# Kernel optimization log

Hardware: AMD Instinct MI355X
Metric: run time of the kernel (lower is better)

## Reference

```python
import jax, jax.numpy as jnp
import numpy as np

N_NODES = 50000
N_EDGES = 800000
N_GRAPHS = 256
VOCAB = 40
EMB = 128
HID = 256
NCLS = 10


def setup_inputs() -> dict:
    key = jax.random.key(0)
    ks = jax.random.split(key, 12)
    x = jax.random.randint(ks[0], (N_NODES,), 0, VOCAB)
    edge_index = jax.random.randint(ks[1], (2, N_EDGES), 0, N_NODES)
    batch = jnp.sort(jax.random.randint(ks[2], (N_NODES,), 0, N_GRAPHS))

    def init(k, shape, fan_in):
        return jax.random.normal(k, shape, jnp.float32) * (1.0 / np.sqrt(fan_in))

    return {
        "x": x,
        "edge_index": edge_index,
        "batch": batch,
        "emb": init(ks[3], (VOCAB, EMB), EMB),
        "W1l": init(ks[4], (EMB, HID), EMB),
        "W1r": init(ks[5], (EMB, HID), EMB),
        "b1": jnp.zeros((HID,), jnp.float32),
        "W2l": init(ks[6], (HID, HID), HID),
        "W2r": init(ks[7], (HID, HID), HID),
        "b2": jnp.zeros((HID,), jnp.float32),
        "Wo": init(ks[8], (HID, NCLS), HID),
        "bo": jnp.zeros((NCLS,), jnp.float32),
    }


def _segment_mean(v, ids, n):
    # v: [M, D], ids: [M] -> [n, D] mean per segment (empty segments -> 0)
    s = jax.ops.segment_sum(v, ids, num_segments=n)
    c = jax.ops.segment_sum(jnp.ones((ids.shape[0], 1), v.dtype), ids, num_segments=n)
    return s / jnp.maximum(c, 1.0)


def _sage_conv(h, src, dst, Wl, Wr, b):
    # PyG SAGEConv: lin_l(mean of neighbor msgs) + lin_r(self) + bias
    mean_nb = _segment_mean(h[src], dst, h.shape[0])  # [N, D_in]
    return mean_nb @ Wl + h @ Wr + b


def reference(x, edge_index, batch, emb, W1l, W1r, b1, W2l, W2r, b2, Wo, bo):
    src, dst = edge_index[0], edge_index[1]
    h = emb[x]                                          # [N, EMB]
    h = jax.nn.relu(_sage_conv(h, src, dst, W1l, W1r, b1))  # [N, HID]
    h = jax.nn.relu(_sage_conv(h, src, dst, W2l, W2r, b2))  # [N, HID]
    g = _segment_mean(h, batch, N_GRAPHS)               # [G, HID]
    return g @ Wo + bo                                  # [G, NCLS]
```

## Files before the change

### kernel.cpp

```cpp
#include <hip/hip_runtime.h>
#include <hip/hip_bf16.h>

#define N_NODES 50000
#define N_GRAPHS 256
#define EMB 128
#define HID 256
#define NCLS 10
#define VOCAB 40
#define NPAD 50048
#define NROW 50048
#define DMAX 64
#define NEDGE 800000
#define P1B 64
#define EPB 12500

typedef __attribute__((ext_vector_type(4))) float f32x4;
typedef __attribute__((ext_vector_type(8))) _Float16 f16x8;
typedef __attribute__((ext_vector_type(4))) _Float16 f16x4;
typedef unsigned int u32;
#define AS1 __attribute__((address_space(1)))
#define AS3 __attribute__((address_space(3)))

__device__ __forceinline__ int imax(int a, int b) { return a > b ? a : b; }
__device__ __forceinline__ int imin(int a, int b) { return a < b ? a : b; }
__device__ __forceinline__ float bf2f(ushort h) { return __uint_as_float(((unsigned)h) << 16); }

__device__ __forceinline__ int detect_bf16(const unsigned short* w) {
    int ok = 1;
#pragma unroll
    for (int i = 0; i < 64; ++i) {
        float f = __uint_as_float(((unsigned)w[i]) << 16);
        ok &= (fabsf(f) < 16.0f) ? 1 : 0;
    }
    return ok;
}
__device__ __forceinline__ float ldw(const void* p, int idx, int bf) {
    if (bf) return bf2f(((const unsigned short*)p)[idx]);
    return ((const float*)p)[idx];
}


struct PrepArgs {
    const void* bsrc[4];
    const unsigned short* emb16;
    const void* W1l; const void* W1r;
    const void* W2l; const void* W2r;
    const int* batch;
    float* Wb;
    _Float16* W2t;
    _Float16* EWt;
    float* EW2;
    int* gstart;
    float* g_acc;
};

__global__ void prep_k(PrepArgs a) {
    int b = blockIdx.x, t = threadIdx.x;
    if (b < 13) {
        int i = b * 256 + t;
        if (i < 3082) {
            int bf = detect_bf16(a.emb16);
            const int cum[5] = {0, 256, 512, 3072, 3082};
            int s = 0;
            while (i >= cum[s + 1]) ++s;
            a.Wb[i] = ldw(a.bsrc[s], i - cum[s], bf);
        }
    } else if (b < 525) {
        int bf = detect_bf16(a.emb16);
        int j = (b - 13) * 256 + t;
        int n = j >> 9, k = j & 511;
        const void* p = (k < 256) ? a.W2l : a.W2r;
        a.W2t[(size_t)n * 512 + k] = (_Float16)ldw(p, (k & 255) * 256 + n, bf);
    } else if (b < 589) {
        int v = b - 525, n = t;
        if (v >= VOCAB) { a.EWt[n * 64 + v] = (_Float16)0.f; return; }
        int bf = detect_bf16(a.emb16);
        float s1 = 0.f, s2 = 0.f;
        for (int k = 0; k < EMB; ++k) {
            float ev = ldw(a.emb16, v * EMB + k, bf);
            s1 = fmaf(ev, ldw(a.W1l, k * 256 + n, bf), s1);
            s2 = fmaf(ev, ldw(a.W1r, k * 256 + n, bf), s2);
        }
        a.EWt[n * 64 + v] = (_Float16)s1;
        a.EW2[v * 256 + n] = s2;
    } else if (b < 785) {
        int i = (b - 589) * 256 + t;
        if (i < N_NODES) {
            int bb = a.batch[i];
            int bp = (i == 0) ? -1 : a.batch[i - 1];
            for (int g = bp + 1; g <= bb; ++g) a.gstart[g] = i;
            if (i == N_NODES - 1)
                for (int g = bb + 1; g <= N_GRAPHS; ++g) a.gstart[g] = N_NODES;
        }
    } else {
        int i = (b - 785) * 256 + t;
        if (i < N_GRAPHS * HID) a.g_acc[i] = 0.f;
    }
}

__global__ __launch_bounds__(1024) void p1_k(const int* __restrict__ dst,
                                             ushort* __restrict__ erank,
                                             ushort* __restrict__ cnts) {
    __shared__ u32 h[NROW / 2];
    int tid = threadIdx.x, blk = blockIdx.x;
    for (int w = tid; w < NROW / 2; w += 1024) h[w] = 0;
    __syncthreads();
    int base = blk * EPB;
    for (int i = tid; i < EPB; i += 1024) {
        int e = base + i;
        int d = dst[e];
        u32 sh = (u32)(d & 1) * 16u;
        u32 old = atomicAdd(&h[d >> 1], 1u << sh);
        erank[e] = (ushort)((old >> sh) & 0xffffu);
    }
    __syncthreads();
    u32* crow = (u32*)(cnts + (size_t)blk * NROW);
    for (int w = tid; w < NROW / 2; w += 1024) crow[w] = h[w];
}

__global__ __launch_bounds__(512) void p2_k(ushort* __restrict__ cnts,
                                            int* __restrict__ deg) {
    __shared__ ushort c[P1B][512];
    int t = threadIdx.x, nb = blockIdx.x * 512;
    int n = nb + t;
    bool ok = (n < NROW);
    for (int b = 0; b < P1B; ++b)
        c[b][t] = ok ? cnts[(size_t)b * NROW + n] : (ushort)0;
    int run = 0;
    for (int b = 0; b < P1B; ++b) {
        int v = c[b][t];
        c[b][t] = (ushort)run;
        run += v;
    }
    if (ok) {
        deg[n] = run;
        for (int b = 0; b < P1B; ++b) cnts[(size_t)b * NROW + n] = c[b][t];
    }
}

__global__ __launch_bounds__(1024) void p3_k(const int* __restrict__ src,
                                             const int* __restrict__ dst,
                                             const ushort* __restrict__ erank,
                                             const ushort* __restrict__ offs,
                                             ushort* __restrict__ col) {
    __shared__ ushort off_l[NROW];
    int tid = threadIdx.x, blk = blockIdx.x;
    const ushort* orow = offs + (size_t)blk * NROW;
    for (int w = tid; w < NROW; w += 1024) off_l[w] = orow[w];
    __syncthreads();
    int base = blk * EPB;
    for (int i = tid; i < EPB; i += 1024) {
        int e = base + i;
        int d = dst[e];
        int p = (int)off_l[d] + (int)erank[e];
        if (p < DMAX) col[(size_t)d * DMAX + p] = (ushort)src[e];
    }
}

__global__ void ct2_k(const int* __restrict__ deg, const ushort* __restrict__ colv,
                      const int* __restrict__ x, char* __restrict__ Ct) {
    __shared__ ushort cnt[VOCAB * 256];
    int tid = threadIdx.x;
    int nl = tid >> 2, sub = tid & 3;
    int n = blockIdx.x * 64 + nl;
#pragma unroll
    for (int v = 0; v < VOCAB; ++v) cnt[v * 256 + tid] = 0;
    if (n < N_NODES) {
        int s0 = n * DMAX;
        int s1 = s0 + imin(deg[n], DMAX);
        for (int e = s0 + sub; e < s1; e += 4) {
            int v = x[colv[e]];
            cnt[v * 256 + tid]++;
        }
    }
    __syncthreads();
    if (tid < 64) {
        int nn = blockIdx.x * 64 + tid;
        char* tile = Ct + (size_t)(nn >> 6) * 8192 + (nn & 63) * 128;
        int xorb = nn & 7;
#pragma unroll
        for (int b = 0; b < 8; ++b) {
            int kbase = (b ^ xorb) * 8;
            f16x8 o;
#pragma unroll
            for (int j = 0; j < 8; ++j) {
                int k = kbase + j;
                int c = 0;
                if (k < VOCAB)
                    c = cnt[k * 256 + tid * 4 + 0] + cnt[k * 256 + tid * 4 + 1] +
                        cnt[k * 256 + tid * 4 + 2] + cnt[k * 256 + tid * 4 + 3];
                o[j] = (_Float16)(float)c;
            }
            *(f16x8*)(tile + b * 16) = o;
        }
    }
}

__global__ __launch_bounds__(256, 2) void gemm1_k(
    const char* __restrict__ Ct, const _Float16* __restrict__ EWt,
    const float* __restrict__ EW2, const int* __restrict__ xv,
    const int* __restrict__ deg, const float* __restrict__ bias,
    char* __restrict__ E) {
    __shared__ __attribute__((aligned(16))) char As[8192];
    const int tid = threadIdx.x, wave = tid >> 6, lane = tid & 63;
    const int row0 = blockIdx.x * 64, col0 = wave * 64;
    const char* sp = Ct + (size_t)blockIdx.x * 8192 + tid * 16;
    __builtin_amdgcn_global_load_lds((const AS1 u32*)sp, (AS3 u32*)(As + tid * 16), 16, 0, 0);
    __builtin_amdgcn_global_load_lds((const AS1 u32*)(sp + 4096),
                                     (AS3 u32*)(As + tid * 16 + 4096), 16, 0, 0);
    f16x8 B[8];
#pragma unroll
    for (int n = 0; n < 4; ++n) {
        const _Float16* wp = EWt + (size_t)(col0 + n * 16 + (lane & 15)) * 64 + ((lane >> 4) * 8);
        B[n] = *(const f16x8*)wp;
        B[4 + n] = *(const f16x8*)(wp + 32);
    }
    int offA[2][4];
#pragma unroll
    for (int h = 0; h < 2; ++h)
#pragma unroll
        for (int m = 0; m < 4; ++m) {
            int r = (lane & 15) + m * 16;
            int b = h * 64 + (lane >> 4) * 16;
            offA[h][m] = r * 128 + (b ^ ((r & 7) << 4));
        }
    f32x4 acc[4][4];
#pragma unroll
    for (int m = 0; m < 4; ++m)
#pragma unroll
        for (int n = 0; n < 4; ++n) acc[m][n] = (f32x4){0.f, 0.f, 0.f, 0.f};
    asm volatile("s_waitcnt vmcnt(0)" ::: "memory");
    __syncthreads();
#pragma unroll
    for (int h = 0; h < 2; ++h) {
        f16x8 a[4];
#pragma unroll
        for (int m = 0; m < 4; ++m) a[m] = *(const f16x8*)(As + offA[h][m]);
#pragma unroll
        for (int m = 0; m < 4; ++m)
#pragma unroll
            for (int n = 0; n < 4; ++n)
                acc[m][n] = __builtin_amdgcn_mfma_f32_16x16x32_f16(a[m], B[h * 4 + n],
                                                                   acc[m][n], 0, 0, 0);
    }
    int rbase = row0 + ((lane >> 4) * 4);
    int cbase = col0 + (lane & 15);
    float bv[4];
#pragma unroll
    for (int n = 0; n < 4; ++n) bv[n] = bias[cbase + n * 16];
#pragma unroll
    for (int m = 0; m < 4; ++m)
#pragma unroll
        for (int r = 0; r < 4; ++r) {
            int row = rbase + m * 16 + r;
            if (row < N_NODES) {
                float invd = 1.f / (float)imax(deg[row], 1);
                const float* e2 = EW2 + (size_t)xv[row] * 256;
#pragma unroll
                for (int n = 0; n < 4; ++n) {
                    int colc = cbase + n * 16;
                    float v = acc[m][n][r] * invd + e2[colc] + bv[n];
                    v = v > 0.f ? v : 0.f;
                    char* ep = E + ((size_t)(row >> 6) * 8 + 4 + (colc >> 6)) * 8192 +
                               (row & 63) * 128 + (((colc & 63) * 2) ^ ((row & 7) << 4));
                    *(_Float16*)ep = (_Float16)v;
                }
            }
        }
}

__global__ void agg2_k(const int* __restrict__ deg, const ushort* __restrict__ colv,
                       char* __restrict__ A2c) {
    int w = (blockIdx.x * blockDim.x + threadIdx.x) >> 6;
    int lane = threadIdx.x & 63;
    if (w >= N_NODES) return;
    int dg = deg[w];
    int s0 = w * DMAX, s1 = s0 + imin(dg, DMAX);
    int ktof = 4 + (lane >> 4);
    int bof = (lane & 15) * 8;
    float ac0 = 0.f, ac1 = 0.f, ac2 = 0.f, ac3 = 0.f;
#define ADDR2(s) (A2c + ((size_t)((s) >> 6) * 8 + ktof) * 8192 + ((s) & 63) * 128 + \
                  (bof ^ (((s) & 7) << 4)))
    int e = s0;
    for (; e + 4 <= s1; e += 4) {
        int sA = colv[e], sB = colv[e + 1], sC = colv[e + 2], sD = colv[e + 3];
        f16x4 h0 = *(const f16x4*)ADDR2(sA);
        f16x4 h1 = *(const f16x4*)ADDR2(sB);
        f16x4 h2 = *(const f16x4*)ADDR2(sC);
        f16x4 h3 = *(const f16x4*)ADDR2(sD);
        ac0 += (float)h0[0] + (float)h1[0] + (float)h2[0] + (float)h3[0];
        ac1 += (float)h0[1] + (float)h1[1] + (float)h2[1] + (float)h3[1];
        ac2 += (float)h0[2] + (float)h1[2] + (float)h2[2] + (float)h3[2];
        ac3 += (float)h0[3] + (float)h1[3] + (float)h2[3] + (float)h3[3];
    }
    for (; e < s1; ++e) {
        f16x4 hv = *(const f16x4*)ADDR2(colv[e]);
        ac0 += (float)hv[0];
        ac1 += (float)hv[1];
        ac2 += (float)hv[2];
        ac3 += (float)hv[3];
    }
#undef ADDR2
    float inv = 1.f / (float)imax(dg, 1);
    f16x4 o;
    o[0] = (_Float16)(ac0 * inv);
    o[1] = (_Float16)(ac1 * inv);
    o[2] = (_Float16)(ac2 * inv);
    o[3] = (_Float16)(ac3 * inv);
    char* mp = A2c + ((size_t)(w >> 6) * 8 + (ktof - 4)) * 8192 + (w & 63) * 128 +
               (bof ^ ((w & 7) << 4));
    *(f16x4*)mp = o;
}

template <int K>
__global__ __launch_bounds__(256, 2) void gemm2_k(
    const char* __restrict__ Aswz, const _Float16* __restrict__ Wt,
    const float* __restrict__ bias, const int* __restrict__ batch,
    float* __restrict__ g_acc) {
    constexpr int NT = K / 64;
    __shared__ __attribute__((aligned(16))) char As[4 * 8192];
    const int tid = threadIdx.x, wave = tid >> 6, lane = tid & 63;
    const int row0 = blockIdx.x * 64, col0 = wave * 64;
    const char* Ab = Aswz + (size_t)blockIdx.x * NT * 8192 + tid * 16;
    const _Float16* Wp = Wt + (size_t)(col0 + (lane & 15)) * K + ((lane >> 4) * 8);

    int offA[2][4];
#pragma unroll
    for (int h = 0; h < 2; ++h)
#pragma unroll
        for (int m = 0; m < 4; ++m) {
            int r = (lane & 15) + m * 16;
            int b = h * 64 + (lane >> 4) * 16;
            offA[h][m] = r * 128 + (b ^ ((r & 7) << 4));
        }

    f32x4 acc[4][4];
#pragma unroll
    for (int m = 0; m < 4; ++m)
#pragma unroll
        for (int n = 0; n < 4; ++n) acc[m][n] = (f32x4){0.f, 0.f, 0.f, 0.f};

    f16x8 B0[8], B1[8];

#define STAGE(t)                                                                     \
    {                                                                                \
        const char* _s = Ab + (size_t)(t) * 8192;                                    \
        char* _d = As + ((t) & 3) * 8192 + tid * 16;                                 \
        __builtin_amdgcn_global_load_lds((const AS1 u32*)_s, (AS3 u32*)_d, 16, 0, 0);\
        __builtin_amdgcn_global_load_lds((const AS1 u32*)(_s + 4096),                \
                                         (AS3 u32*)(_d + 4096), 16, 0, 0);           \
    }
#define LOADB(t, Bf)                                                                 \
    {                                                                                \
        _Pragma("unroll") for (int n = 0; n < 4; ++n) {                              \
            Bf[n]     = *(const f16x8*)(Wp + (size_t)n * 16 * K + (t) * 64);         \
            Bf[4 + n] = *(const f16x8*)(Wp + (size_t)n * 16 * K + (t) * 64 + 32);    \
        }                                                                            \
    }
#define COMP(p, Bf)                                                                  \
    {                                                                                \
        const char* _b = As + (p) * 8192;                                            \
        _Pragma("unroll") for (int h = 0; h < 2; ++h) {                              \
            f16x8 _a[4];                                                             \
            _Pragma("unroll") for (int m = 0; m < 4; ++m)                            \
                _a[m] = *(const f16x8*)(_b + offA[h][m]);                            \
            _Pragma("unroll") for (int m = 0; m < 4; ++m)                            \
                _Pragma("unroll") for (int n = 0; n < 4; ++n)                        \
                    acc[m][n] = __builtin_amdgcn_mfma_f32_16x16x32_f16(              \
                        _a[m], Bf[h * 4 + n], acc[m][n], 0, 0, 0);                   \
        }                                                                            \
    }
#define WAITBAR()                                                                    \
    {                                                                                \
        asm volatile("s_waitcnt vmcnt(12)" ::: "memory");                            \
        __builtin_amdgcn_s_barrier();                                                \
        asm volatile("" ::: "memory");                                               \
    }

    STAGE(0);
    LOADB(0, B0);
    STAGE(1);
    STAGE(2);

#pragma unroll 1
    for (int t = 0; t < NT; t += 2) {
        WAITBAR();
        if (t + 3 < NT) STAGE(t + 3);
        LOADB(t + 1, B1);
        COMP(t & 3, B0);
        WAITBAR();
        if (t + 4 < NT) STAGE(t + 4);
        if (t + 2 < NT) LOADB(t + 2, B0);
        COMP((t + 1) & 3, B1);
    }

    __syncthreads();
    float bv[4];
#pragma unroll
    for (int n = 0; n < 4; ++n) bv[n] = bias[col0 + n * 16 + (lane & 15)];
    int rloc = (lane >> 4) * 4;
    int cbase = col0 + (lane & 15);
#pragma unroll
    for (int m = 0; m < 4; ++m)
#pragma unroll
        for (int n = 0; n < 4; ++n)
#pragma unroll
            for (int r = 0; r < 4; ++r) {
                float v = acc[m][n][r] + bv[n];
                v = v > 0.f ? v : 0.f;
                *(_Float16*)(As + (rloc + m * 16 + r) * 512 + (cbase + n * 16) * 2) =
                    (_Float16)v;
            }
    __syncthreads();
    int rmax = imin(64, N_NODES - row0);
    int cur = batch[row0];
    float run = 0.f;
    for (int r = 0; r < rmax; ++r) {
        int b = batch[row0 + r];
        if (b != cur) {
            atomicAdd(&g_acc[cur * HID + tid], run);
            run = 0.f;
            cur = b;
        }
        run += (float)*(const _Float16*)(As + r * 512 + tid * 2);
    }
    atomicAdd(&g_acc[cur * HID + tid], run);
#undef STAGE
#undef LOADB
#undef COMP
#undef WAITBAR
}

__global__ void final_k(const float* __restrict__ g_acc, const int* __restrict__ gstart,
                        const float* __restrict__ Wo, const float* __restrict__ bo,
                        void* __restrict__ out, const unsigned short* __restrict__ emb16) {
    __shared__ float gm[HID];
    __shared__ float red[HID];
    int g = blockIdx.x, t = threadIdx.x;
    int cnt = gstart[g + 1] - gstart[g];
    float inv = 1.0f / (float)imax(cnt, 1);
    gm[t] = g_acc[g * HID + t] * inv;
    __syncthreads();
    int bf = detect_bf16(emb16);
    for (int c = 0; c < NCLS; ++c) {
        red[t] = gm[t] * Wo[t * NCLS + c];
        __syncthreads();
        for (int s = HID / 2; s > 0; s >>= 1) {
            if (t < s) red[t] += red[t + s];
            __syncthreads();
        }
        if (t == 0) {
            float o = red[0] + bo[c];
            if (bf) ((__hip_bfloat16*)out)[g * NCLS + c] = __float2bfloat16(o);
            else    ((float*)out)[g * NCLS + c] = o;
        }
        __syncthreads();
    }
}

extern "C" void kernel_launch(void* const* d_in, const int* in_sizes, int n_in,
                              void* d_out, int out_size, void* d_ws, size_t ws_size,
                              hipStream_t stream) {
    const int* x     = (const int*)d_in[0];
    const int* ei    = (const int*)d_in[1];
    const int* batch = (const int*)d_in[2];
    const int* srcp = ei;
    const int* dstp = ei + NEDGE;

    char* w = (char*)d_ws;
    auto alloc = [&](size_t bytes) -> char* {
        char* p = w;
        w += (bytes + 255) & ~(size_t)255;
        return p;
    };
    float* g_acc = (float*)alloc((size_t)N_GRAPHS * HID * 4);
    int* deg     = (int*)alloc((size_t)NROW * 4);
    int* gstart  = (int*)alloc((size_t)(N_GRAPHS + 1) * 4);
    ushort* erank = (ushort*)alloc((size_t)NEDGE * 2);
    ushort* cnts  = (ushort*)alloc((size_t)P1B * NROW * 2);
    ushort* col   = (ushort*)alloc((size_t)N_NODES * DMAX * 2);
    float* Wb     = (float*)alloc((size_t)3328 * 4);
    _Float16* W2t = (_Float16*)alloc((size_t)256 * 512 * 2);
    _Float16* EWt = (_Float16*)alloc((size_t)256 * 64 * 2);
    float* EW2    = (float*)alloc((size_t)VOCAB * 256 * 4);
    char* Ct      = alloc((size_t)(NPAD / 64) * 8192);
    char* A2c     = alloc((size_t)(NPAD / 64) * 8 * 8192);
    alloc(4096);

    PrepArgs pa;
    pa.bsrc[0] = d_in[6];  pa.bsrc[1] = d_in[9];
    pa.bsrc[2] = d_in[10]; pa.bsrc[3] = d_in[11];
    pa.emb16 = (const unsigned short*)d_in[3];
    pa.W1l = d_in[4]; pa.W1r = d_in[5];
    pa.W2l = d_in[7]; pa.W2r = d_in[8];
    pa.batch = batch;
    pa.Wb = Wb; pa.W2t = W2t; pa.EWt = EWt; pa.EW2 = EW2;
    pa.gstart = gstart; pa.g_acc = g_acc;
    prep_k<<<1041, 256, 0, stream>>>(pa);

    p1_k<<<P1B, 1024, 0, stream>>>(dstp, erank, cnts);
    p2_k<<<(NROW + 511) / 512, 512, 0, stream>>>(cnts, deg);
    p3_k<<<P1B, 1024, 0, stream>>>(srcp, dstp, erank, cnts, col);

    const int GB = NPAD / 64;
    ct2_k<<<GB, 256, 0, stream>>>(deg, col, x, Ct);
    gemm1_k<<<GB, 256, 0, stream>>>(Ct, EWt, EW2, x, deg, Wb, A2c);
    agg2_k<<<(N_NODES * 64 + 255) / 256, 256, 0, stream>>>(deg, col, A2c);
    gemm2_k<512><<<GB, 256, 0, stream>>>(A2c, W2t, Wb + 256, batch, g_acc);
    final_k<<<N_GRAPHS, HID, 0, stream>>>(g_acc, gstart, Wb + 512, Wb + 3072, d_out,
                                          (const unsigned short*)d_in[3]);

    (void)in_sizes; (void)n_in; (void)out_size; (void)ws_size;
}
```

Measured before the change: 221.1 us.

## Replace multi-pass CSR build with atomic scatter and fuse vocab counts into gemm1

The three-kernel build of the neighbor lists (per-block histogram, prefix scan, placement) is replaced by one kernel. It uses a global atomicAdd on each node's degree to claim a slot and write the source id directly. The vocab-count kernel is merged into gemm1, so the count tile is built in LDS and consumed there without a global round trip. This removes three launches and the erank/cnts/Ct buffers. The cost is contended global atomics and a nondeterministic neighbor order.

```diff
diff --git a/kernel.cpp b/kernel.cpp
--- a/kernel.cpp
+++ b/kernel.cpp
@@ -8,11 +8,8 @@
 #define NCLS 10
 #define VOCAB 40
 #define NPAD 50048
-#define NROW 50048
 #define DMAX 64
 #define NEDGE 800000
-#define P1B 64
-#define EPB 12500
 
 typedef __attribute__((ext_vector_type(4))) float f32x4;
 typedef __attribute__((ext_vector_type(8))) _Float16 f16x8;
@@ -52,6 +49,7 @@
     float* EW2;
     int* gstart;
     float* g_acc;
+    int* deg;
 };
 
 __global__ void prep_k(PrepArgs a) {
@@ -92,79 +90,48 @@
             if (i == N_NODES - 1)
                 for (int g = bb + 1; g <= N_GRAPHS; ++g) a.gstart[g] = N_NODES;
         }
-    } else {
+    } else if (b < 1041) {
         int i = (b - 785) * 256 + t;
         if (i < N_GRAPHS * HID) a.g_acc[i] = 0.f;
-    }
-}
-
-__global__ __launch_bounds__(1024) void p1_k(const int* __restrict__ dst,
-                                             ushort* __restrict__ erank,
-                                             ushort* __restrict__ cnts) {
-    __shared__ u32 h[NROW / 2];
-    int tid = threadIdx.x, blk = blockIdx.x;
-    for (int w = tid; w < NROW / 2; w += 1024) h[w] = 0;
-    __syncthreads();
-    int base = blk * EPB;
-    for (int i = tid; i < EPB; i += 1024) {
-        int e = base + i;
+    } else {
+        int i = (b - 1041) * 256 + t;
+        if (i < N_NODES) a.deg[i] = 0;
+    }
+}
+
+__global__ void scatter_k(const int* __restrict__ src, const int* __restrict__ dst,
+                          int* __restrict__ deg, ushort* __restrict__ col) {
+    int e = blockIdx.x * blockDim.x + threadIdx.x;
+    if (e < NEDGE) {
         int d = dst[e];
-        u32 sh = (u32)(d & 1) * 16u;
-        u32 old = atomicAdd(&h[d >> 1], 1u << sh);
-        erank[e] = (ushort)((old >> sh) & 0xffffu);
-    }
-    __syncthreads();
-    u32* crow = (u32*)(cnts + (size_t)blk * NROW);
-    for (int w = tid; w < NROW / 2; w += 1024) crow[w] = h[w];
-}
-
-__global__ __launch_bounds__(512) void p2_k(ushort* __restrict__ cnts,
-                                            int* __restrict__ deg) {
-    __shared__ ushort c[P1B][512];
-    int t = threadIdx.x, nb = blockIdx.x * 512;
-    int n = nb + t;
-    bool ok = (n < NROW);
-    for (int b = 0; b < P1B; ++b)
-        c[b][t] = ok ? cnts[(size_t)b * NROW + n] : (ushort)0;
-    int run = 0;
-    for (int b = 0; b < P1B; ++b) {
-        int v = c[b][t];
-        c[b][t] = (ushort)run;
-        run += v;
-    }
-    if (ok) {
-        deg[n] = run;
-        for (int b = 0; b < P1B; ++b) cnts[(size_t)b * NROW + n] = c[b][t];
-    }
-}
-
-__global__ __launch_bounds__(1024) void p3_k(const int* __restrict__ src,
-                                             const int* __restrict__ dst,
-                                             const ushort* __restrict__ erank,
-                                             const ushort* __restrict__ offs,
-                                             ushort* __restrict__ col) {
-    __shared__ ushort off_l[NROW];
-    int tid = threadIdx.x, blk = blockIdx.x;
-    const ushort* orow = offs + (size_t)blk * NROW;
-    for (int w = tid; w < NROW; w += 1024) off_l[w] = orow[w];
-    __syncthreads();
-    int base = blk * EPB;
-    for (int i = tid; i < EPB; i += 1024) {
-        int e = base + i;
-        int d = dst[e];
-        int p = (int)off_l[d] + (int)erank[e];
-        if (p < DMAX) col[(size_t)d * DMAX + p] = (ushort)src[e];
-    }
-}
-
-__global__ void ct2_k(const int* __restrict__ deg, const ushort* __restrict__ colv,
-                      const int* __restrict__ x, char* __restrict__ Ct) {
+        int p = atomicAdd(&deg[d], 1);
+        if (p < DMAX) col[d * DMAX + p] = (ushort)src[e];
+    }
+}
+
+__global__ __launch_bounds__(256, 2) void gemm1_k(
+    const int* __restrict__ deg, const ushort* __restrict__ colv,
+    const int* __restrict__ x, const _Float16* __restrict__ EWt,
+    const float* __restrict__ EW2, const float* __restrict__ bias,
+    char* __restrict__ E) {
     __shared__ ushort cnt[VOCAB * 256];
-    int tid = threadIdx.x;
+    __shared__ __attribute__((aligned(16))) char As[8192];
+    const int tid = threadIdx.x, wave = tid >> 6, lane = tid & 63;
+    const int row0 = blockIdx.x * 64, col0 = wave * 64;
+
+    f16x8 B[8];
+#pragma unroll
+    for (int n = 0; n < 4; ++n) {
+        const _Float16* wp = EWt + (size_t)(col0 + n * 16 + (lane & 15)) * 64 + ((lane >> 4) * 8);
+        B[n] = *(const f16x8*)wp;
+        B[4 + n] = *(const f16x8*)(wp + 32);
+    }
+
     int nl = tid >> 2, sub = tid & 3;
-    int n = blockIdx.x * 64 + nl;
+    int n = row0 + nl;
 #pragma unroll
     for (int v = 0; v < VOCAB; ++v) cnt[v * 256 + tid] = 0;
+    __syncthreads();
     if (n < N_NODES) {
         int s0 = n * DMAX;
         int s1 = s0 + imin(deg[n], DMAX);
@@ -175,9 +142,8 @@
     }
     __syncthreads();
     if (tid < 64) {
-        int nn = blockIdx.x * 64 + tid;
-        char* tile = Ct + (size_t)(nn >> 6) * 8192 + (nn & 63) * 128;
-        int xorb = nn & 7;
+        char* trow = As + tid * 128;
+        int xorb = tid & 7;
 #pragma unroll
         for (int b = 0; b < 8; ++b) {
             int kbase = (b ^ xorb) * 8;
@@ -191,30 +157,11 @@
                         cnt[k * 256 + tid * 4 + 2] + cnt[k * 256 + tid * 4 + 3];
                 o[j] = (_Float16)(float)c;
             }
-            *(f16x8*)(tile + b * 16) = o;
-        }
-    }
-}
-
-__global__ __launch_bounds__(256, 2) void gemm1_k(
-    const char* __restrict__ Ct, const _Float16* __restrict__ EWt,
-    const float* __restrict__ EW2, const int* __restrict__ xv,
-    const int* __restrict__ deg, const float* __restrict__ bias,
-    char* __restrict__ E) {
-    __shared__ __attribute__((aligned(16))) char As[8192];
-    const int tid = threadIdx.x, wave = tid >> 6, lane = tid & 63;
-    const int row0 = blockIdx.x * 64, col0 = wave * 64;
-    const char* sp = Ct + (size_t)blockIdx.x * 8192 + tid * 16;
-    __builtin_amdgcn_global_load_lds((const AS1 u32*)sp, (AS3 u32*)(As + tid * 16), 16, 0, 0);
-    __builtin_amdgcn_global_load_lds((const AS1 u32*)(sp + 4096),
-                                     (AS3 u32*)(As + tid * 16 + 4096), 16, 0, 0);
-    f16x8 B[8];
-#pragma unroll
-    for (int n = 0; n < 4; ++n) {
-        const _Float16* wp = EWt + (size_t)(col0 + n * 16 + (lane & 15)) * 64 + ((lane >> 4) * 8);
-        B[n] = *(const f16x8*)wp;
-        B[4 + n] = *(const f16x8*)(wp + 32);
-    }
+            *(f16x8*)(trow + b * 16) = o;
+        }
+    }
+    __syncthreads();
+
     int offA[2][4];
 #pragma unroll
     for (int h = 0; h < 2; ++h)
@@ -228,9 +175,7 @@
 #pragma unroll
     for (int m = 0; m < 4; ++m)
 #pragma unroll
-        for (int n = 0; n < 4; ++n) acc[m][n] = (f32x4){0.f, 0.f, 0.f, 0.f};
-    asm volatile("s_waitcnt vmcnt(0)" ::: "memory");
-    __syncthreads();
+        for (int nn = 0; nn < 4; ++nn) acc[m][nn] = (f32x4){0.f, 0.f, 0.f, 0.f};
 #pragma unroll
     for (int h = 0; h < 2; ++h) {
         f16x8 a[4];
@@ -239,15 +184,15 @@
 #pragma unroll
         for (int m = 0; m < 4; ++m)
 #pragma unroll
-            for (int n = 0; n < 4; ++n)
-                acc[m][n] = __builtin_amdgcn_mfma_f32_16x16x32_f16(a[m], B[h * 4 + n],
-                                                                   acc[m][n], 0, 0, 0);
+            for (int nn = 0; nn < 4; ++nn)
+                acc[m][nn] = __builtin_amdgcn_mfma_f32_16x16x32_f16(a[m], B[h * 4 + nn],
+                                                                    acc[m][nn], 0, 0, 0);
     }
     int rbase = row0 + ((lane >> 4) * 4);
     int cbase = col0 + (lane & 15);
     float bv[4];
 #pragma unroll
-    for (int n = 0; n < 4; ++n) bv[n] = bias[cbase + n * 16];
+    for (int nn = 0; nn < 4; ++nn) bv[nn] = bias[cbase + nn * 16];
 #pragma unroll
     for (int m = 0; m < 4; ++m)
 #pragma unroll
@@ -255,11 +200,11 @@
             int row = rbase + m * 16 + r;
             if (row < N_NODES) {
                 float invd = 1.f / (float)imax(deg[row], 1);
-                const float* e2 = EW2 + (size_t)xv[row] * 256;
-#pragma unroll
-                for (int n = 0; n < 4; ++n) {
-                    int colc = cbase + n * 16;
-                    float v = acc[m][n][r] * invd + e2[colc] + bv[n];
+                const float* e2 = EW2 + (size_t)x[row] * 256;
+#pragma unroll
+                for (int nn = 0; nn < 4; ++nn) {
+                    int colc = cbase + nn * 16;
+                    float v = acc[m][nn][r] * invd + e2[colc] + bv[nn];
                     v = v > 0.f ? v : 0.f;
                     char* ep = E + ((size_t)(row >> 6) * 8 + 4 + (colc >> 6)) * 8192 +
                                (row & 63) * 128 + (((colc & 63) * 2) ^ ((row & 7) << 4));
@@ -474,16 +419,13 @@
         return p;
     };
     float* g_acc = (float*)alloc((size_t)N_GRAPHS * HID * 4);
-    int* deg     = (int*)alloc((size_t)NROW * 4);
+    int* deg     = (int*)alloc((size_t)N_NODES * 4);
     int* gstart  = (int*)alloc((size_t)(N_GRAPHS + 1) * 4);
-    ushort* erank = (ushort*)alloc((size_t)NEDGE * 2);
-    ushort* cnts  = (ushort*)alloc((size_t)P1B * NROW * 2);
-    ushort* col   = (ushort*)alloc((size_t)N_NODES * DMAX * 2);
-    float* Wb     = (float*)alloc((size_t)3328 * 4);
+    ushort* col  = (ushort*)alloc((size_t)N_NODES * DMAX * 2);
+    float* Wb    = (float*)alloc((size_t)3328 * 4);
     _Float16* W2t = (_Float16*)alloc((size_t)256 * 512 * 2);
     _Float16* EWt = (_Float16*)alloc((size_t)256 * 64 * 2);
     float* EW2    = (float*)alloc((size_t)VOCAB * 256 * 4);
-    char* Ct      = alloc((size_t)(NPAD / 64) * 8192);
     char* A2c     = alloc((size_t)(NPAD / 64) * 8 * 8192);
     alloc(4096);
 
@@ -495,16 +437,13 @@
     pa.W2l = d_in[7]; pa.W2r = d_in[8];
     pa.batch = batch;
     pa.Wb = Wb; pa.W2t = W2t; pa.EWt = EWt; pa.EW2 = EW2;
-    pa.gstart = gstart; pa.g_acc = g_acc;
-    prep_k<<<1041, 256, 0, stream>>>(pa);
-
-    p1_k<<<P1B, 1024, 0, stream>>>(dstp, erank, cnts);
-    p2_k<<<(NROW + 511) / 512, 512, 0, stream>>>(cnts, deg);
-    p3_k<<<P1B, 1024, 0, stream>>>(srcp, dstp, erank, cnts, col);
+    pa.gstart = gstart; pa.g_acc = g_acc; pa.deg = deg;
+    prep_k<<<1237, 256, 0, stream>>>(pa);
+
+    scatter_k<<<(NEDGE + 255) / 256, 256, 0, stream>>>(srcp, dstp, deg, col);
 
     const int GB = NPAD / 64;
-    ct2_k<<<GB, 256, 0, stream>>>(deg, col, x, Ct);
-    gemm1_k<<<GB, 256, 0, stream>>>(Ct, EWt, EW2, x, deg, Wb, A2c);
+    gemm1_k<<<GB, 256, 0, stream>>>(deg, col, x, EWt, EW2, Wb, A2c);
     agg2_k<<<(N_NODES * 64 + 255) / 256, 256, 0, stream>>>(deg, col, A2c);
     gemm2_k<512><<<GB, 256, 0, stream>>>(A2c, W2t, Wb + 256, batch, g_acc);
     final_k<<<N_GRAPHS, HID, 0, stream>>>(g_acc, gstart, Wb + 512, Wb + 3072, d_out,
```

Result: faster. 208.9 us (-5.5%).
